# Performance work log

Hardware: AMD Instinct MI355X
Metric: run time of the kernel (lower is better)

Reference implementation:

```python
import jax, jax.numpy as jnp
import numpy as np

N, E, VD, HD, ES = 10000, 80000, 32, 64, 68
NET_IN = VD * VD + 2 * HD + ES   # 1220: f2s(1024) + s[e0](64) + s[e1](64) + edge_s(68)
SELF_IN = VD * VD + 2 * HD       # 1152: temp_f2s(1024) + s(64) + s_c(64)
OUT_D = VD * VD + HD             # 1088: vector channel mixer + scalar update


def _lecun(k, fin, fout):
    return jax.random.normal(k, (fin, fout), jnp.float32) / jnp.sqrt(jnp.float32(fin))


def setup_inputs() -> dict:
    ks = jax.random.split(jax.random.key(0), 16)
    return {
        "f": jax.random.normal(ks[0], (N, 3, VD), jnp.float32),
        "s": jax.random.normal(ks[1], (N, HD), jnp.float32),
        "edge_f": jax.random.normal(ks[2], (E, 3, 1), jnp.float32),
        "edge_s": jax.random.normal(ks[3], (E, ES), jnp.float32),
        "W_emb1": _lecun(ks[4], 2 * VD + 1, VD),
        "net_W1": _lecun(ks[5], NET_IN, HD), "net_b1": jnp.zeros((HD,), jnp.float32),
        "net_W2": _lecun(ks[6], HD, HD), "net_b2": jnp.zeros((HD,), jnp.float32),
        "net_W3": _lecun(ks[7], HD, OUT_D), "net_b3": jnp.zeros((OUT_D,), jnp.float32),
        "W_emb2": _lecun(ks[8], 2 * VD, VD),
        "self_W1": _lecun(ks[9], SELF_IN, HD), "self_b1": jnp.zeros((HD,), jnp.float32),
        "self_W2": _lecun(ks[10], HD, HD), "self_b2": jnp.zeros((HD,), jnp.float32),
        "self_W3": _lecun(ks[11], HD, OUT_D), "self_b3": jnp.zeros((OUT_D,), jnp.float32),
        "edge_index": jax.random.randint(ks[12], (2, E), 0, N),
    }


def _mlp(x, W1, b1, W2, b2, W3, b3):
    h = jax.nn.relu(x @ W1 + b1)
    h = jax.nn.relu(h @ W2 + b2)
    return h @ W3 + b3


def _segment_mean(x, ids, n):
    tot = jax.ops.segment_sum(x, ids, num_segments=n)
    cnt = jax.ops.segment_sum(jnp.ones(ids.shape, x.dtype), ids, num_segments=n)
    return tot / jnp.maximum(cnt, 1.0).reshape((n,) + (1,) * (x.ndim - 1))


def _forward(f, s, edge_f, edge_s,
             W_emb1, net_W1, net_b1, net_W2, net_b2, net_W3, net_b3,
             W_emb2, self_W1, self_b1, self_W2, self_b2, self_W3, self_b3,
             edge_index):
    n = f.shape[0]
    e0, e1 = edge_index[0], edge_index[1]
    # --- edge message: gather -> embed -> gram einsum -> MLP ---
    _f = jnp.concatenate((f[e0], f[e1], edge_f), axis=-1)          # [E,3,2VD+1]
    _s = jnp.concatenate((s[e0], s[e1], edge_s), axis=-1)          # [E,2HD+ES]
    _f = _f @ W_emb1                                               # [E,3,VD]
    f2s = jnp.einsum('eij,eik->ejk', _f, _f).reshape(-1, VD * VD)  # _f^T @ _f, [E,VD*VD]
    Fn = jnp.linalg.norm(f2s, axis=-1, keepdims=True) + 1.0
    c = _mlp(jnp.concatenate((f2s, _s), axis=-1),
             net_W1, net_b1, net_W2, net_b2, net_W3, net_b3) / Fn  # [E,OUT_D]
    f_c = jnp.einsum('eij,ejk->eik', _f, c[:, :VD * VD].reshape(-1, VD, VD))  # [E,3,VD]
    f_c = _segment_mean(f_c, e0, n)                                # [N,3,VD]
    s_c = _segment_mean(c[:, VD * VD:], e0, n)                     # [N,HD]
    # --- node self-update ---
    tf = jnp.concatenate((f, f_c), axis=-1) @ W_emb2               # [N,3,VD]
    tf2s = jnp.einsum('nij,nik->njk', tf, tf).reshape(n, VD * VD)
    Fn2 = jnp.linalg.norm(tf2s, axis=-1, keepdims=True) + 1.0
    c2 = _mlp(jnp.concatenate((tf2s, s, s_c), axis=-1),
              self_W1, self_b1, self_W2, self_b2, self_W3, self_b3) / Fn2
    f_out = jnp.einsum('nij,njk->nik', tf, c2[:, :VD * VD].reshape(-1, VD, VD)) + f
    s_out = c2[:, VD * VD:] + s
    return f_out, s_out


def reference(f, s, edge_f, edge_s,
              W_emb1, net_W1, net_b1, net_W2, net_b2, net_W3, net_b3,
              W_emb2, self_W1, self_b1, self_W2, self_b2, self_W3, self_b3,
              edge_index):
    return _forward(f, s, edge_f, edge_s,
                    W_emb1, net_W1, net_b1, net_W2, net_b2, net_W3, net_b3,
                    W_emb2, self_W1, self_b1, self_W2, self_b2, self_W3, self_b3,
                    edge_index)
```

## Files before the change

### kernel.cpp

```cpp
#include <hip/hip_runtime.h>
#include <math.h>

#define NN 10000
#define NE 80000
#define SFH 102
#define SFB 98
#define SSB 66
#define STX 72
#define NTRI 528
#define SAE 104
#define SAN 72

typedef __attribute__((ext_vector_type(8))) __bf16 bf16x8;
typedef __attribute__((ext_vector_type(8))) short short8v;
typedef __attribute__((ext_vector_type(4))) float f32x4;
typedef __attribute__((ext_vector_type(4))) unsigned uint4v;

__device__ __forceinline__ ushort f2bf(float x) {
  union { float f; unsigned u; } v; v.f = x;
  unsigned r = v.u + 0x7FFFu + ((v.u >> 16) & 1u);
  return (ushort)(r >> 16);
}
__device__ __forceinline__ float bfu(ushort u) {
  union { unsigned x; float f; } v; v.x = (unsigned)u << 16;
  return v.f;
}
__device__ __forceinline__ void tri_ab(int k, int& a, int& b) {
  int aa = 0, rem = k;
  while (rem >= 32 - aa) { rem -= 32 - aa; ++aa; }
  a = aa; b = aa + rem;
}

__global__ __launch_bounds__(1024)
void sgnn_scan(const int* __restrict__ deg, int* __restrict__ cursor,
               int* __restrict__ start) {
  __shared__ int sm[1024];
  const int t = threadIdx.x;
  const int i0 = t * 10;
  int v[10], pre = 0;
  #pragma unroll
  for (int q = 0; q < 10; ++q) {
    const int i = i0 + q;
    v[q] = (i < NN) ? deg[i] : 0;
    pre += v[q];
  }
  sm[t] = pre;
  __syncthreads();
  int run = pre;
  #pragma unroll
  for (int d = 1; d < 1024; d <<= 1) {
    const int add = (t >= d) ? sm[t - d] : 0;
    __syncthreads();
    run += add;
    sm[t] = run;
    __syncthreads();
  }
  int excl = run - pre;
  #pragma unroll
  for (int q = 0; q < 10; ++q) {
    const int i = i0 + q;
    if (i < NN) { cursor[i] = excl; start[i] = excl; }
    excl += v[q];
  }
}

__global__ __launch_bounds__(256)
void sgnn_scatter(const int* __restrict__ eidx, int* __restrict__ cursor,
                  int* __restrict__ sorted) {
  const int e = blockIdx.x * 256 + threadIdx.x;
  if (e < NE) {
    const int p = atomicAdd(cursor + eidx[e], 1);
    sorted[p] = e;
  }
}

__global__ __launch_bounds__(256)
void sgnn_wconv(const float* __restrict__ nW1, const float* __restrict__ nW2,
                const float* __restrict__ nW3, const float* __restrict__ sW1,
                const float* __restrict__ sW2, const float* __restrict__ sW3,
                const float* __restrict__ Wemb1, const float* __restrict__ Wemb2,
                const int* __restrict__ eidx, int* __restrict__ deg,
                ushort* __restrict__ wout, ushort* __restrict__ tab) {
  const int gid = blockIdx.x * 256 + threadIdx.x;
  if (gid < NE) atomicAdd(deg + eidx[gid], 1);
  if (gid >= 61 * 4096) {
    const int k = gid - 61 * 4096;
    if (k < NTRI) {
      int a, b; tri_ab(k, a, b);
      tab[k] = (ushort)(a | (b << 8) | ((a != b) ? 0x8000 : 0));
    }
    return;
  }
  const int tile = gid >> 12, idx = gid & 4095;
  const int c = idx >> 6, k = idx & 63;
  float v = 0.f;
  if (tile < 12) {
    const int T = tile;
    if (T < 8 || (T == 8 && k < 16)) {
      const int ktri = T * 64 + k;
      if (ktri < NTRI) {
        int a, b; tri_ab(ktri, a, b);
        v = nW1[(a * 32 + b) * 64 + c];
        if (a != b) v += nW1[(b * 32 + a) * 64 + c];
      }
    } else if (T == 8) { if (k < 20) v = nW1[(1216 + (k - 16)) * 64 + c]; }
    else if (T == 9)   v = nW1[(1024 + k) * 64 + c];
    else if (T == 10)  v = nW1[(1088 + k) * 64 + c];
    else               v = nW1[(1152 + k) * 64 + c];
  } else if (tile == 12) v = nW2[k * 64 + c];
  else if (tile < 30)    v = nW3[k * 1088 + (tile - 13) * 64 + c];
  else if (tile < 41) {
    const int T = tile - 30;
    if (T < 8 || (T == 8 && k < 16)) {
      const int ktri = T * 64 + k;
      if (ktri < NTRI) {
        int a, b; tri_ab(ktri, a, b);
        v = sW1[(a * 32 + b) * 64 + c];
        if (a != b) v += sW1[(b * 32 + a) * 64 + c];
      }
    } else if (T == 9) v = sW1[(1024 + k) * 64 + c];
    else if (T == 10)  v = sW1[(1088 + k) * 64 + c];
  } else if (tile == 41) v = sW2[k * 64 + c];
  else if (tile < 59)    v = sW3[k * 1088 + (tile - 42) * 64 + c];
  else if (tile == 59) {
    const int col = idx / 96, kk = idx % 96;
    v = (col < 32 && kk < 65) ? Wemb1[kk * 32 + col] : 0.f;
  } else {
    const int col = idx >> 6;
    v = (col < 32) ? Wemb2[k * 32 + col] : 0.f;
  }
  wout[gid] = f2bf(v);
}

#define STAGE_W(srcbase) do { const ushort* _s = (srcbase);                      \
  _Pragma("unroll") for (int rr = 0; rr < 2; ++rr) {                             \
    const int idx_ = t + 256 * rr; const int c_ = idx_ >> 3, ko_ = idx_ & 7;     \
    *(short8v*)&Wl[c_ * STX + ko_ * 8] = *(const short8v*)&_s[c_ * 64 + ko_ * 8];\
  } } while (0)

#define WPRE_LOAD(srcbase) do { const ushort* _s = (srcbase);                    \
  wpre0 = *(const short8v*)&_s[(t >> 3) * 64 + (t & 7) * 8];                     \
  wpre1 = *(const short8v*)&_s[(32 + (t >> 3)) * 64 + (t & 7) * 8]; } while (0)

#define WPRE_STORE() do {                                                        \
  *(short8v*)&Wl[(t >> 3) * STX + (t & 7) * 8] = wpre0;                          \
  *(short8v*)&Wl[(32 + (t >> 3)) * STX + (t & 7) * 8] = wpre1; } while (0)

#define MFMA_K64() do {                                                          \
  _Pragma("unroll") for (int kb = 0; kb < 2; ++kb) {                             \
    const bf16x8 af_ = *(const bf16x8*)&Xl[(w * 16 + ll) * STX + kb * 32 + lh * 8]; \
    acc[0] = __builtin_amdgcn_mfma_f32_16x16x32_bf16(af_,                        \
        *(const bf16x8*)&Wl[(     ll) * STX + kb * 32 + lh * 8], acc[0], 0, 0, 0); \
    acc[1] = __builtin_amdgcn_mfma_f32_16x16x32_bf16(af_,                        \
        *(const bf16x8*)&Wl[(16 + ll) * STX + kb * 32 + lh * 8], acc[1], 0, 0, 0); \
    acc[2] = __builtin_amdgcn_mfma_f32_16x16x32_bf16(af_,                        \
        *(const bf16x8*)&Wl[(32 + ll) * STX + kb * 32 + lh * 8], acc[2], 0, 0, 0); \
    acc[3] = __builtin_amdgcn_mfma_f32_16x16x32_bf16(af_,                        \
        *(const bf16x8*)&Wl[(48 + ll) * STX + kb * 32 + lh * 8], acc[3], 0, 0, 0); \
  } } while (0)

#define ZERO_ACC() do { _Pragma("unroll") for (int q = 0; q < 4; ++q)            \
    acc[q] = (f32x4){0.f, 0.f, 0.f, 0.f}; } while (0)

#define PACK_STORE16(dstp) do {                                                  \
  unsigned pk[8];                                                                \
  _Pragma("unroll") for (int q = 0; q < 8; ++q)                                  \
    pk[q] = (unsigned)f2bf(xv[2 * q]) | ((unsigned)f2bf(xv[2 * q + 1]) << 16);   \
  *(uint4v*)(dstp)       = (uint4v){pk[0], pk[1], pk[2], pk[3]};                 \
  *(uint4v*)((dstp) + 8) = (uint4v){pk[4], pk[5], pk[6], pk[7]};                 \
} while (0)

#define TRI16(kt) do {                                                           \
  int prev_a = -1; float fa0 = 0.f, fa1 = 0.f, fa2 = 0.f;                        \
  _Pragma("unroll") for (int m = 0; m < 16; ++m) {                               \
    const int tb = tabL[(kt) + m];                                               \
    const int a_ = tb & 31, b_ = (tb >> 8) & 31;                                 \
    if (a_ != prev_a) { fa0 = bfu(fr[a_]); fa1 = bfu(fr[32 + a_]);               \
                        fa2 = bfu(fr[64 + a_]); prev_a = a_; }                   \
    const float v = fmaf(fa0, bfu(fr[b_]),                                       \
        fmaf(fa1, bfu(fr[32 + b_]), fa2 * bfu(fr[64 + b_])));                    \
    const float wsel = (tb & 0x8000) ? 2.f : 1.f;                                \
    sumsq = fmaf(v * wsel, v, sumsq);                                            \
    xv[m] = v;                                                                   \
  } } while (0)

#define XV_LOAD16(p) do { const float* _p = (p);                                 \
  _Pragma("unroll") for (int q = 0; q < 4; ++q) {                                \
    const float4 v4 = *(const float4*)(_p + 4 * q);                              \
    xv[4 * q + 0] = v4.x; xv[4 * q + 1] = v4.y;                                  \
    xv[4 * q + 2] = v4.z; xv[4 * q + 3] = v4.w; } } while (0)

#define CONSUME_NT() do {                                                        \
  _Pragma("unroll") for (int r = 0; r < 4; ++r) {                                \
    const int row_ = w * 16 + lh * 4 + r;                                        \
    const unsigned u0 = *(const unsigned*)&smFh[row_ * SFH +      nt * 2];       \
    const unsigned u1 = *(const unsigned*)&smFh[row_ * SFH + 32 + nt * 2];       \
    const unsigned u2 = *(const unsigned*)&smFh[row_ * SFH + 64 + nt * 2];       \
    union { unsigned x; float f; } l0, h0, l1, h1, l2, h2;                       \
    l0.x = u0 << 16; h0.x = u0 & 0xffff0000u;                                    \
    l1.x = u1 << 16; h1.x = u1 & 0xffff0000u;                                    \
    l2.x = u2 << 16; h2.x = u2 & 0xffff0000u;                                    \
    _Pragma("unroll") for (int nc = 0; nc < 4; ++nc) {                           \
      const float cv = (acc[nc][r] + b3v[nc]) * ifnr[r];                         \
      const int p = nc & 1;                                                      \
      const float f0 = (nc < 2) ? l0.f : h0.f;                                   \
      const float f1 = (nc < 2) ? l1.f : h1.f;                                   \
      const float f2 = (nc < 2) ? l2.f : h2.f;                                   \
      fch[(r * 3 + 0) * 2 + p] = fmaf(f0, cv, fch[(r * 3 + 0) * 2 + p]);         \
      fch[(r * 3 + 1) * 2 + p] = fmaf(f1, cv, fch[(r * 3 + 1) * 2 + p]);         \
      fch[(r * 3 + 2) * 2 + p] = fmaf(f2, cv, fch[(r * 3 + 2) * 2 + p]);         \
    }                                                                            \
  } } while (0)

#define STAGE_FS() do {                                                          \
  _Pragma("unroll") for (int r = 0; r < 4; ++r) {                                \
    const int row_ = w * 16 + lh * 4 + r;                                        \
    _Pragma("unroll") for (int i = 0; i < 3; ++i) {                              \
      F[row_ * SFB + i * 32 + ll]      = f2bf(fch[(r * 3 + i) * 2 + 0]);         \
      F[row_ * SFB + i * 32 + ll + 16] = f2bf(fch[(r * 3 + i) * 2 + 1]);         \
    }                                                                            \
    _Pragma("unroll") for (int nc = 0; nc < 4; ++nc)                             \
      S[row_ * SSB + nc * 16 + ll] = f2bf(cs[nc * 4 + r]);                       \
  } } while (0)

#define LDS_BYTES 34656

__global__ __launch_bounds__(256, 3)
void sgnn_edge(const float* __restrict__ f, const float* __restrict__ s,
               const float* __restrict__ edge_f, const float* __restrict__ edge_s,
               const float* __restrict__ b1, const float* __restrict__ b2,
               const float* __restrict__ b3,
               const ushort* __restrict__ wbf, const ushort* __restrict__ tab_g,
               const int* __restrict__ eidx, const int* __restrict__ sorted,
               const int* __restrict__ start_g, const int* __restrict__ deg_g,
               float* __restrict__ fc_sum, float* __restrict__ sc_sum) {
  __shared__ __align__(16) char sbuf[LDS_BYTES];
  ushort* smFh = (ushort*)sbuf;
  ushort* F    = (ushort*)sbuf;
  ushort* Xl   = (ushort*)(sbuf + 13056);
  ushort* S    = (ushort*)(sbuf + 13056);
  ushort* Aemb = (ushort*)(sbuf + 13056);
  ushort* Wl   = (ushort*)(sbuf + 22272);
  float*  red  = (float*)(sbuf + 31488);
  int*    snode = (int*)(sbuf + 31488);
  int*    srow0 = snode + 8;
  int*    srow1 = snode + 16;
  int*    sst   = snode + 24;
  int*    sdg   = snode + 32;
  ushort* tabL = (ushort*)(sbuf + 33088);
  float*  iFn  = (float*)(sbuf + 33088);
  int*    es_s = (int*)(sbuf + 34144);
  ushort* e0s  = (ushort*)(sbuf + 34400);
  ushort* e1s  = (ushort*)(sbuf + 34528);

  const int t = threadIdx.x, j = t & 63, w = t >> 6, eb = w * 16;
  const int lh = j >> 4, ll = j & 15;
  const int bid = blockIdx.x;
  const ushort* wembT = wbf + 59 * 4096;
  short8v wpre0, wpre1;

  if (t < 64) {
    const int e = sorted[bid * 64 + t];
    es_s[t] = e;
    e0s[t] = (ushort)eidx[e];
    e1s[t] = (ushort)eidx[NE + e];
  }
  for (int idx = t; idx < NTRI; idx += 256) tabL[idx] = tab_g[idx];
  __syncthreads();

  int str = 0, dgr = 0;
  if (j < 16) {
    const int n_ = e0s[eb + j];
    str = start_g[n_];
    dgr = deg_g[n_];
  }
  WPRE_LOAD(wbf + 0);

  #pragma unroll 1
  for (int h = 0; h < 2; ++h) {
    const int hb = h * 32;
    #pragma unroll 1
    for (int cc = t; cc < 576; cc += 256) {
      const int row = cc / 6, seg = cc - row * 6;
      const int lel = (row * 43) >> 7, il = row - lel * 3;
      const int k0 = seg * 16;
      float xv[16];
      if (seg < 4) {
        const int nd = (seg < 2) ? (int)e0s[hb + lel] : (int)e1s[hb + lel];
        XV_LOAD16(f + nd * 96 + il * 32 + (seg & 1) * 16);
      } else if (seg == 4) {
        xv[0] = edge_f[es_s[hb + lel] * 3 + il];
        #pragma unroll
        for (int m = 1; m < 16; ++m) xv[m] = 0.f;
      } else {
        #pragma unroll
        for (int m = 0; m < 16; ++m) xv[m] = 0.f;
      }
      PACK_STORE16(&Aemb[row * SAE + k0]);
    }
    __syncthreads();
    #pragma unroll 1
    for (int job = w * 3; job < w * 3 + 3; ++job) {
      const int mt = job >> 1, nt = job & 1;
      f32x4 ac = (f32x4){0.f, 0.f, 0.f, 0.f};
      #pragma unroll
      for (int kb = 0; kb < 3; ++kb) {
        const bf16x8 av = *(const bf16x8*)&Aemb[(mt * 16 + ll) * SAE + kb * 32 + lh * 8];
        const bf16x8 bv = *(const bf16x8*)&wembT[(nt * 16 + ll) * 96 + kb * 32 + lh * 8];
        ac = __builtin_amdgcn_mfma_f32_16x16x32_bf16(av, bv, ac, 0, 0, 0);
      }
      #pragma unroll
      for (int r = 0; r < 4; ++r) {
        const int rr = mt * 16 + lh * 4 + r;
        const int lel = (rr * 43) >> 7, il = rr - lel * 3;
        smFh[(hb + lel) * SFH + il * 32 + nt * 16 + ll] = f2bf(ac[r]);
      }
    }
    __syncthreads();
  }

  f32x4 acc[4];
  ZERO_ACC();
  float sumsq = 0.f;

  #pragma unroll 1
  for (int T = 0; T < 12; ++T) {
    __syncthreads();
    WPRE_STORE();
    {
      const ushort* fr = smFh + j * SFH;
      float xv[16];
      if (T < 8) {
        TRI16(T * 64 + w * 16);
      } else if (T == 8) {
        if (w == 0) {
          TRI16(512);
        } else if (w == 1) {
          const float4 v4 = *(const float4*)(edge_s + es_s[j] * 68 + 64);
          xv[0] = v4.x; xv[1] = v4.y; xv[2] = v4.z; xv[3] = v4.w;
          #pragma unroll
          for (int m = 4; m < 16; ++m) xv[m] = 0.f;
        } else {
          #pragma unroll
          for (int m = 0; m < 16; ++m) xv[m] = 0.f;
        }
      } else if (T == 9)  { XV_LOAD16(s + e0s[j] * 64 + w * 16); }
      else if (T == 10)   { XV_LOAD16(s + e1s[j] * 64 + w * 16); }
      else                { XV_LOAD16(edge_s + es_s[j] * 68 + w * 16); }
      PACK_STORE16(&Xl[j * STX + w * 16]);
    }
    __syncthreads();
    WPRE_LOAD(wbf + (T + 1) * 4096);
    MFMA_K64();
  }

  __syncthreads();
  red[w * 64 + j] = sumsq;
  #pragma unroll
  for (int nc = 0; nc < 4; ++nc) {
    const float bv = b1[nc * 16 + ll];
    #pragma unroll
    for (int r = 0; r < 4; ++r)
      Xl[(w * 16 + lh * 4 + r) * STX + nc * 16 + ll] = f2bf(fmaxf(acc[nc][r] + bv, 0.f));
  }
  WPRE_STORE();
  ZERO_ACC();
  __syncthreads();
  if (t < 64) {
    const float ss = red[t] + red[64 + t] + red[128 + t] + red[192 + t];
    iFn[t] = 1.f / (sqrtf(ss) + 1.f);
  }

  MFMA_K64();
  #pragma unroll
  for (int nc = 0; nc < 4; ++nc) {
    const float bv = b2[nc * 16 + ll];
    #pragma unroll
    for (int r = 0; r < 4; ++r)
      Xl[(w * 16 + lh * 4 + r) * STX + nc * 16 + ll] = f2bf(fmaxf(acc[nc][r] + bv, 0.f));
  }

  float fch[24];
  #pragma unroll
  for (int q = 0; q < 24; ++q) fch[q] = 0.f;
  float cs[16];
  float ifnr[4];

  #pragma unroll 1
  for (int nt = 0; nt < 17; ++nt) {
    __syncthreads();
    STAGE_W(wbf + (13 + nt) * 4096);
    float b3v[4];
    #pragma unroll
    for (int nc = 0; nc < 4; ++nc) b3v[nc] = b3[nt * 64 + nc * 16 + ll];
    __syncthreads();
    if (nt == 0) {
      #pragma unroll
      for (int r = 0; r < 4; ++r) ifnr[r] = iFn[w * 16 + lh * 4 + r];
    }
    ZERO_ACC();
    MFMA_K64();
    if (nt < 16) {
      CONSUME_NT();
    } else {
      #pragma unroll
      for (int nc = 0; nc < 4; ++nc)
        #pragma unroll
        for (int r = 0; r < 4; ++r)
          cs[nc * 4 + r] = (acc[nc][r] + b3v[nc]) * ifnr[r];
    }
  }

  __syncthreads();
  STAGE_FS();
  if (t < 8) snode[t] = -1;
  __syncthreads();

  {
    float r0 = 0.f, r1 = 0.f, rs = 0.f;
    int runlen = 0;
    const int gwb = bid * 64 + eb;
    #pragma unroll 1
    for (int m = 0; m < 16; ++m) {
      const int row = eb + m;
      r0 += bfu(F[row * SFB + j]);
      if (j < 32) r1 += bfu(F[row * SFB + 64 + j]);
      rs += bfu(S[row * SSB + j]);
      ++runlen;
      const int n = e0s[row];
      if (m == 15 || e0s[row + 1] != n) {
        const int st = __shfl(str, m);
        const int dg = __shfl(dgr, m);
        const int g1v = gwb + m, g0v = g1v - runlen + 1;
        if (g0v == st && runlen == dg) {
          fc_sum[n * 96 + j] = r0;
          if (j < 32) fc_sum[n * 96 + 64 + j] = r1;
          sc_sum[n * 64 + j] = rs;
        } else {
          const int slot = (g0v == gwb) ? 2 * w : 2 * w + 1;
          if (j == 0) {
            snode[slot] = n; srow0[slot] = row - runlen + 1; srow1[slot] = row;
            sst[slot] = st; sdg[slot] = dg;
          }
        }
        r0 = r1 = rs = 0.f; runlen = 0;
      }
    }
  }
  __syncthreads();

  if (t < 160) {
    const int ch = t;
    int prevn = -1;
    #pragma unroll 1
    for (int ss = 0; ss < 8; ++ss) {
      const int n = snode[ss];
      if (n < 0) continue;
      if (n != prevn) {
        float v = 0.f;
        #pragma unroll 1
        for (int k2 = ss; k2 < 8; ++k2) {
          if (snode[k2] == n) {
            #pragma unroll 1
            for (int row = srow0[k2]; row <= srow1[k2]; ++row)
              v += (ch < 96) ? bfu(F[row * SFB + ch]) : bfu(S[row * SSB + (ch - 96)]);
          } else if (k2 > ss && snode[k2] >= 0) break;
        }
        const bool cib = (sst[ss] >= bid * 64) && (sst[ss] + sdg[ss] <= bid * 64 + 64);
        float* dst = (ch < 96) ? (fc_sum + n * 96 + ch) : (sc_sum + n * 64 + (ch - 96));
        if (cib) *dst = v; else atomicAdd(dst, v);
      }
      prevn = n;
    }
  }
}

__global__ __launch_bounds__(256, 3)
void sgnn_node(const float* __restrict__ f, const float* __restrict__ s,
               const float* __restrict__ b1, const float* __restrict__ b2,
               const float* __restrict__ b3,
               const ushort* __restrict__ wbf, const ushort* __restrict__ tab_g,
               const float* __restrict__ fcm, const float* __restrict__ scm,
               const int* __restrict__ deg_g,
               float* __restrict__ of, float* __restrict__ os) {
  __shared__ __align__(16) char sbuf[LDS_BYTES];
  ushort* smFh = (ushort*)sbuf;
  ushort* F    = (ushort*)sbuf;
  ushort* Xl   = (ushort*)(sbuf + 13056);
  ushort* S    = (ushort*)(sbuf + 13056);
  ushort* Aemb = (ushort*)(sbuf + 13056);
  ushort* Wl   = (ushort*)(sbuf + 22272);
  float*  red  = (float*)(sbuf + 31488);
  float*  icntL = (float*)(sbuf + 31488);
  ushort* tabL = (ushort*)(sbuf + 33088);
  float*  iFn  = (float*)(sbuf + 33088);

  const int t = threadIdx.x, j = t & 63, w = t >> 6, eb = w * 16;
  const int lh = j >> 4, ll = j & 15;
  const int nbase = blockIdx.x * 64;
  const ushort* wembTn = wbf + 60 * 4096;
  short8v wpre0, wpre1;

  for (int idx = t; idx < NTRI; idx += 256) tabL[idx] = tab_g[idx];
  if (t < 64)
    icntL[t] = 1.f / fmaxf((float)deg_g[min(nbase + t, NN - 1)], 1.f);
  WPRE_LOAD(wbf + 30 * 4096);
  __syncthreads();

  #pragma unroll 1
  for (int h = 0; h < 2; ++h) {
    const int hb = h * 32;
    #pragma unroll 1
    for (int cc = t; cc < 384; cc += 256) {
      const int row = cc >> 2, seg = cc & 3;
      const int lel = (row * 43) >> 7, il = row - lel * 3;
      const int nc = min(nbase + hb + lel, NN - 1);
      const int k0 = seg * 16;
      float xv[16];
      if (seg < 2) {
        XV_LOAD16(f + nc * 96 + il * 32 + seg * 16);
      } else {
        XV_LOAD16(fcm + nc * 96 + il * 32 + (seg - 2) * 16);
        const float ic = icntL[hb + lel];
        #pragma unroll
        for (int m = 0; m < 16; ++m) xv[m] *= ic;
      }
      PACK_STORE16(&Aemb[row * SAN + k0]);
    }
    __syncthreads();
    #pragma unroll 1
    for (int job = w * 3; job < w * 3 + 3; ++job) {
      const int mt = job >> 1, nt = job & 1;
      f32x4 ac = (f32x4){0.f, 0.f, 0.f, 0.f};
      #pragma unroll
      for (int kb = 0; kb < 2; ++kb) {
        const bf16x8 av = *(const bf16x8*)&Aemb[(mt * 16 + ll) * SAN + kb * 32 + lh * 8];
        const bf16x8 bv = *(const bf16x8*)&wembTn[(nt * 16 + ll) * 64 + kb * 32 + lh * 8];
        ac = __builtin_amdgcn_mfma_f32_16x16x32_bf16(av, bv, ac, 0, 0, 0);
      }
      #pragma unroll
      for (int r = 0; r < 4; ++r) {
        const int rr = mt * 16 + lh * 4 + r;
        const int lel = (rr * 43) >> 7, il = rr - lel * 3;
        smFh[(hb + lel) * SFH + il * 32 + nt * 16 + ll] = f2bf(ac[r]);
      }
    }
    __syncthreads();
  }

  f32x4 acc[4];
  ZERO_ACC();
  float sumsq = 0.f;

  #pragma unroll 1
  for (int T = 0; T < 11; ++T) {
    __syncthreads();
    WPRE_STORE();
    {
      const ushort* fr = smFh + j * SFH;
      float xv[16];
      if (T < 8) {
        TRI16(T * 64 + w * 16);
      } else if (T == 8) {
        if (w == 0) {
          TRI16(512);
        } else {
          #pragma unroll
          for (int m = 0; m < 16; ++m) xv[m] = 0.f;
        }
      } else if (T == 9) {
        XV_LOAD16(s + min(nbase + j, NN - 1) * 64 + w * 16);
      } else {
        XV_LOAD16(scm + min(nbase + j, NN - 1) * 64 + w * 16);
        const float ic = icntL[j];
        #pragma unroll
        for (int m = 0; m < 16; ++m) xv[m] *= ic;
      }
      PACK_STORE16(&Xl[j * STX + w * 16]);
    }
    __syncthreads();
    WPRE_LOAD(wbf + (31 + T) * 4096);
    MFMA_K64();
  }

  __syncthreads();
  red[w * 64 + j] = sumsq;
  #pragma unroll
  for (int nc = 0; nc < 4; ++nc) {
    const float bv = b1[nc * 16 + ll];
    #pragma unroll
    for (int r = 0; r < 4; ++r)
      Xl[(w * 16 + lh * 4 + r) * STX + nc * 16 + ll] = f2bf(fmaxf(acc[nc][r] + bv, 0.f));
  }
  WPRE_STORE();
  ZERO_ACC();
  __syncthreads();
  if (t < 64) {
    const float ss = red[t] + red[64 + t] + red[128 + t] + red[192 + t];
    iFn[t] = 1.f / (sqrtf(ss) + 1.f);
  }

  MFMA_K64();
  #pragma unroll
  for (int nc = 0; nc < 4; ++nc) {
    const float bv = b2[nc * 16 + ll];
    #pragma unroll
    for (int r = 0; r < 4; ++r)
      Xl[(w * 16 + lh * 4 + r) * STX + nc * 16 + ll] = f2bf(fmaxf(acc[nc][r] + bv, 0.f));
  }

  float fch[24];
  #pragma unroll
  for (int q = 0; q < 24; ++q) fch[q] = 0.f;
  float cs[16];
  float ifnr[4];

  #pragma unroll 1
  for (int nt = 0; nt < 17; ++nt) {
    __syncthreads();
    STAGE_W(wbf + (42 + nt) * 4096);
    float b3v[4];
    #pragma unroll
    for (int nc = 0; nc < 4; ++nc) b3v[nc] = b3[nt * 64 + nc * 16 + ll];
    __syncthreads();
    if (nt == 0) {
      #pragma unroll
      for (int r = 0; r < 4; ++r) ifnr[r] = iFn[w * 16 + lh * 4 + r];
    }
    ZERO_ACC();
    MFMA_K64();
    if (nt < 16) {
      CONSUME_NT();
    } else {
      #pragma unroll
      for (int nc = 0; nc < 4; ++nc)
        #pragma unroll
        for (int r = 0; r < 4; ++r)
          cs[nc * 4 + r] = (acc[nc][r] + b3v[nc]) * ifnr[r];
    }
  }

  __syncthreads();
  STAGE_FS();
  __syncthreads();

  #pragma unroll 1
  for (int m = 0; m < 16; ++m) {
    const int row = eb + m;
    const int n_m = nbase + row;
    if (n_m < NN) {
      of[n_m * 96 + j] = bfu(F[row * SFB + j]) + f[n_m * 96 + j];
      if (j < 32)
        of[n_m * 96 + 64 + j] = bfu(F[row * SFB + 64 + j]) + f[n_m * 96 + 64 + j];
      os[n_m * 64 + j] = bfu(S[row * SSB + j]) + s[n_m * 64 + j];
    }
  }
}

extern "C" void kernel_launch(void* const* d_in, const int* in_sizes, int n_in,
                              void* d_out, int out_size, void* d_ws, size_t ws_size,
                              hipStream_t stream) {
  const float* f      = (const float*)d_in[0];
  const float* s      = (const float*)d_in[1];
  const float* edge_f = (const float*)d_in[2];
  const float* edge_s = (const float*)d_in[3];
  const float* Wemb1  = (const float*)d_in[4];
  const float* nW1 = (const float*)d_in[5];
  const float* nb1 = (const float*)d_in[6];
  const float* nW2 = (const float*)d_in[7];
  const float* nb2 = (const float*)d_in[8];
  const float* nW3 = (const float*)d_in[9];
  const float* nb3 = (const float*)d_in[10];
  const float* Wemb2 = (const float*)d_in[11];
  const float* sW1 = (const float*)d_in[12];
  const float* sb1 = (const float*)d_in[13];
  const float* sW2 = (const float*)d_in[14];
  const float* sb2 = (const float*)d_in[15];
  const float* sW3 = (const float*)d_in[16];
  const float* sb3 = (const float*)d_in[17];
  const int* eidx  = (const int*)d_in[18];

  float* of = (float*)d_out;
  float* os = of + (size_t)NN * 96;

  int* deg    = (int*)d_ws;
  int* cursor = deg + NN;
  int* start  = cursor + NN;
  int* sorted = start + NN;
  ushort* wbf = (ushort*)(sorted + NE);
  ushort* tab = wbf + 61 * 4096;

  hipMemsetAsync(deg, 0, (size_t)NN * 4, stream);
  hipMemsetAsync(d_out, 0, (size_t)NN * 160 * 4, stream);

  hipLaunchKernelGGL(sgnn_wconv, dim3((61 * 4096 + NTRI + 255) / 256), dim3(256),
                     0, stream, nW1, nW2, nW3, sW1, sW2, sW3, Wemb1, Wemb2,
                     eidx, deg, wbf, tab);
  hipLaunchKernelGGL(sgnn_scan, dim3(1), dim3(1024), 0, stream, deg, cursor, start);
  hipLaunchKernelGGL(sgnn_scatter, dim3((NE + 255) / 256), dim3(256), 0, stream,
                     eidx, cursor, sorted);
  hipLaunchKernelGGL(sgnn_edge, dim3(NE / 64), dim3(256), 0, stream,
                     f, s, edge_f, edge_s, nb1, nb2, nb3,
                     wbf, tab, eidx, sorted, start, deg,
                     of , os );
  hipLaunchKernelGGL(sgnn_node, dim3((NN + 63) / 64), dim3(256), 0, stream,
                     f, s, sb1, sb2, sb3,
                     wbf, tab, of , os , deg, of, os);
}
```

Baseline: 202.3 us.

## Build MFMA A-operands in registers and prefetch layer-3 weights

In both the edge and node kernels, each lane now computes the gram features for exactly the slots of its MFMA A-fragment and packs them straight into bf16x8 registers. This drops the per-tile store of activations to the Xl shared-memory tile and the reads back from it. The sum-of-squares reduction for the norm becomes a wave shuffle instead of a shared-memory reduction. The third-layer weight staging switches from synchronous STAGE_W to register prefetch (WPRE_LOAD/STORE) one tile ahead, so global weight loads overlap the MFMAs. The cost is higher register pressure at launch bounds of 3 blocks per SM, and recomputation of the repeated frA loads.

```diff
diff --git a/kernel.cpp b/kernel.cpp
--- a/kernel.cpp
+++ b/kernel.cpp
@@ -146,6 +146,25 @@
   *(short8v*)&Wl[(t >> 3) * STX + (t & 7) * 8] = wpre0;                          \
   *(short8v*)&Wl[(32 + (t >> 3)) * STX + (t & 7) * 8] = wpre1; } while (0)
 
+#define MFMA_K64_RA() do {                                                       \
+  acc[0] = __builtin_amdgcn_mfma_f32_16x16x32_bf16(af0.v8,                       \
+      *(const bf16x8*)&Wl[(     ll) * STX + lh * 8], acc[0], 0, 0, 0);           \
+  acc[1] = __builtin_amdgcn_mfma_f32_16x16x32_bf16(af0.v8,                       \
+      *(const bf16x8*)&Wl[(16 + ll) * STX + lh * 8], acc[1], 0, 0, 0);           \
+  acc[2] = __builtin_amdgcn_mfma_f32_16x16x32_bf16(af0.v8,                       \
+      *(const bf16x8*)&Wl[(32 + ll) * STX + lh * 8], acc[2], 0, 0, 0);           \
+  acc[3] = __builtin_amdgcn_mfma_f32_16x16x32_bf16(af0.v8,                       \
+      *(const bf16x8*)&Wl[(48 + ll) * STX + lh * 8], acc[3], 0, 0, 0);           \
+  acc[0] = __builtin_amdgcn_mfma_f32_16x16x32_bf16(af1.v8,                       \
+      *(const bf16x8*)&Wl[(     ll) * STX + 32 + lh * 8], acc[0], 0, 0, 0);      \
+  acc[1] = __builtin_amdgcn_mfma_f32_16x16x32_bf16(af1.v8,                       \
+      *(const bf16x8*)&Wl[(16 + ll) * STX + 32 + lh * 8], acc[1], 0, 0, 0);      \
+  acc[2] = __builtin_amdgcn_mfma_f32_16x16x32_bf16(af1.v8,                       \
+      *(const bf16x8*)&Wl[(32 + ll) * STX + 32 + lh * 8], acc[2], 0, 0, 0);      \
+  acc[3] = __builtin_amdgcn_mfma_f32_16x16x32_bf16(af1.v8,                       \
+      *(const bf16x8*)&Wl[(48 + ll) * STX + 32 + lh * 8], acc[3], 0, 0, 0);      \
+} while (0)
+
 #define MFMA_K64() do {                                                          \
   _Pragma("unroll") for (int kb = 0; kb < 2; ++kb) {                             \
     const bf16x8 af_ = *(const bf16x8*)&Xl[(w * 16 + ll) * STX + kb * 32 + lh * 8]; \
@@ -170,19 +189,32 @@
   *(uint4v*)((dstp) + 8) = (uint4v){pk[4], pk[5], pk[6], pk[7]};                 \
 } while (0)
 
-#define TRI16(kt) do {                                                           \
+#define PACK_AF() do {                                                           \
+  _Pragma("unroll") for (int q2 = 0; q2 < 4; ++q2) {                             \
+    af0.u[q2] = (unsigned)f2bf(xv[2 * q2]) | ((unsigned)f2bf(xv[2 * q2 + 1]) << 16); \
+    af1.u[q2] = (unsigned)f2bf(xv[8 + 2 * q2]) | ((unsigned)f2bf(xv[8 + 2 * q2 + 1]) << 16); \
+  } } while (0)
+
+#define TRI8(kt, off) do {                                                       \
   int prev_a = -1; float fa0 = 0.f, fa1 = 0.f, fa2 = 0.f;                        \
-  _Pragma("unroll") for (int m = 0; m < 16; ++m) {                               \
-    const int tb = tabL[(kt) + m];                                               \
+  _Pragma("unroll") for (int q = 0; q < 8; ++q) {                                \
+    const int tb = tabL[(kt) + q];                                               \
     const int a_ = tb & 31, b_ = (tb >> 8) & 31;                                 \
-    if (a_ != prev_a) { fa0 = bfu(fr[a_]); fa1 = bfu(fr[32 + a_]);               \
-                        fa2 = bfu(fr[64 + a_]); prev_a = a_; }                   \
-    const float v = fmaf(fa0, bfu(fr[b_]),                                       \
-        fmaf(fa1, bfu(fr[32 + b_]), fa2 * bfu(fr[64 + b_])));                    \
+    if (a_ != prev_a) { fa0 = bfu(frA[a_]); fa1 = bfu(frA[32 + a_]);             \
+                        fa2 = bfu(frA[64 + a_]); prev_a = a_; }                  \
+    const float v = fmaf(fa0, bfu(frA[b_]),                                      \
+        fmaf(fa1, bfu(frA[32 + b_]), fa2 * bfu(frA[64 + b_])));                  \
     const float wsel = (tb & 0x8000) ? 2.f : 1.f;                                \
     sumsq = fmaf(v * wsel, v, sumsq);                                            \
-    xv[m] = v;                                                                   \
+    xv[(off) + q] = v;                                                           \
   } } while (0)
+
+#define XV8_LOAD(p, off) do { const float* _p = (p);                             \
+  const float4 va = *(const float4*)(_p);                                        \
+  const float4 vb = *(const float4*)(_p + 4);                                    \
+  xv[(off)+0]=va.x; xv[(off)+1]=va.y; xv[(off)+2]=va.z; xv[(off)+3]=va.w;        \
+  xv[(off)+4]=vb.x; xv[(off)+5]=vb.y; xv[(off)+6]=vb.z; xv[(off)+7]=vb.w;        \
+} while (0)
 
 #define XV_LOAD16(p) do { const float* _p = (p);                                 \
   _Pragma("unroll") for (int q = 0; q < 4; ++q) {                                \
@@ -241,7 +273,6 @@
   ushort* S    = (ushort*)(sbuf + 13056);
   ushort* Aemb = (ushort*)(sbuf + 13056);
   ushort* Wl   = (ushort*)(sbuf + 22272);
-  float*  red  = (float*)(sbuf + 31488);
   int*    snode = (int*)(sbuf + 31488);
   int*    srow0 = snode + 8;
   int*    srow1 = snode + 16;
@@ -322,40 +353,58 @@
   f32x4 acc[4];
   ZERO_ACC();
   float sumsq = 0.f;
+  const int rowA = w * 16 + ll;
+  const ushort* frA = smFh + rowA * SFH;
 
   #pragma unroll 1
   for (int T = 0; T < 12; ++T) {
+    float xv[16];
+    union { unsigned u[4]; bf16x8 v8; } af0, af1;
+    if (T < 8) {
+      TRI8(T * 64 + lh * 8, 0);
+      TRI8(T * 64 + 32 + lh * 8, 8);
+    } else if (T == 8) {
+      #pragma unroll
+      for (int kb2 = 0; kb2 < 2; ++kb2)
+        #pragma unroll
+        for (int q = 0; q < 8; ++q) {
+          const int k = kb2 * 32 + lh * 8 + q;
+          float v = 0.f;
+          if (k < 16) {
+            const int tb = tabL[512 + k];
+            const int a_ = tb & 31, b_ = (tb >> 8) & 31;
+            v = fmaf(bfu(frA[a_]), bfu(frA[b_]),
+                fmaf(bfu(frA[32 + a_]), bfu(frA[32 + b_]),
+                     bfu(frA[64 + a_]) * bfu(frA[64 + b_])));
+            const float wsel = (tb & 0x8000) ? 2.f : 1.f;
+            sumsq = fmaf(v * wsel, v, sumsq);
+          } else if (k < 20) {
+            v = edge_s[es_s[rowA] * 68 + 64 + (k - 16)];
+          }
+          xv[kb2 * 8 + q] = v;
+        }
+    } else {
+      const float* p = (T == 9)  ? (s + e0s[rowA] * 64)
+                     : (T == 10) ? (s + e1s[rowA] * 64)
+                                 : (edge_s + es_s[rowA] * 68);
+      XV8_LOAD(p + lh * 8, 0);
+      XV8_LOAD(p + 32 + lh * 8, 8);
+    }
+    PACK_AF();
     __syncthreads();
     WPRE_STORE();
-    {
-      const ushort* fr = smFh + j * SFH;
-      float xv[16];
-      if (T < 8) {
-        TRI16(T * 64 + w * 16);
-      } else if (T == 8) {
-        if (w == 0) {
-          TRI16(512);
-        } else if (w == 1) {
-          const float4 v4 = *(const float4*)(edge_s + es_s[j] * 68 + 64);
-          xv[0] = v4.x; xv[1] = v4.y; xv[2] = v4.z; xv[3] = v4.w;
-          #pragma unroll
-          for (int m = 4; m < 16; ++m) xv[m] = 0.f;
-        } else {
-          #pragma unroll
-          for (int m = 0; m < 16; ++m) xv[m] = 0.f;
-        }
-      } else if (T == 9)  { XV_LOAD16(s + e0s[j] * 64 + w * 16); }
-      else if (T == 10)   { XV_LOAD16(s + e1s[j] * 64 + w * 16); }
-      else                { XV_LOAD16(edge_s + es_s[j] * 68 + w * 16); }
-      PACK_STORE16(&Xl[j * STX + w * 16]);
-    }
     __syncthreads();
     WPRE_LOAD(wbf + (T + 1) * 4096);
-    MFMA_K64();
-  }
-
-  __syncthreads();
-  red[w * 64 + j] = sumsq;
+    MFMA_K64_RA();
+  }
+
+  {
+    float ss = sumsq;
+    ss += __shfl_xor(ss, 16);
+    ss += __shfl_xor(ss, 32);
+    __syncthreads();
+    if (j < 16) iFn[eb + j] = 1.f / (sqrtf(ss) + 1.f);
+  }
   #pragma unroll
   for (int nc = 0; nc < 4; ++nc) {
     const float bv = b1[nc * 16 + ll];
@@ -366,10 +415,7 @@
   WPRE_STORE();
   ZERO_ACC();
   __syncthreads();
-  if (t < 64) {
-    const float ss = red[t] + red[64 + t] + red[128 + t] + red[192 + t];
-    iFn[t] = 1.f / (sqrtf(ss) + 1.f);
-  }
+  WPRE_LOAD(wbf + 13 * 4096);
 
   MFMA_K64();
   #pragma unroll
@@ -389,11 +435,12 @@
   #pragma unroll 1
   for (int nt = 0; nt < 17; ++nt) {
     __syncthreads();
-    STAGE_W(wbf + (13 + nt) * 4096);
+    WPRE_STORE();
     float b3v[4];
     #pragma unroll
     for (int nc = 0; nc < 4; ++nc) b3v[nc] = b3[nt * 64 + nc * 16 + ll];
     __syncthreads();
+    if (nt < 16) WPRE_LOAD(wbf + (14 + nt) * 4096);
     if (nt == 0) {
       #pragma unroll
       for (int r = 0; r < 4; ++r) ifnr[r] = iFn[w * 16 + lh * 4 + r];
@@ -490,7 +537,6 @@
   ushort* S    = (ushort*)(sbuf + 13056);
   ushort* Aemb = (ushort*)(sbuf + 13056);
   ushort* Wl   = (ushort*)(sbuf + 22272);
-  float*  red  = (float*)(sbuf + 31488);
   float*  icntL = (float*)(sbuf + 31488);
   ushort* tabL = (ushort*)(sbuf + 33088);
   float*  iFn  = (float*)(sbuf + 33088);
@@ -551,40 +597,60 @@
   f32x4 acc[4];
   ZERO_ACC();
   float sumsq = 0.f;
+  const int rowA = w * 16 + ll;
+  const ushort* frA = smFh + rowA * SFH;
+  const int ncA = min(nbase + rowA, NN - 1);
 
   #pragma unroll 1
   for (int T = 0; T < 11; ++T) {
+    float xv[16];
+    union { unsigned u[4]; bf16x8 v8; } af0, af1;
+    if (T < 8) {
+      TRI8(T * 64 + lh * 8, 0);
+      TRI8(T * 64 + 32 + lh * 8, 8);
+    } else if (T == 8) {
+      #pragma unroll
+      for (int kb2 = 0; kb2 < 2; ++kb2)
+        #pragma unroll
+        for (int q = 0; q < 8; ++q) {
+          const int k = kb2 * 32 + lh * 8 + q;
+          float v = 0.f;
+          if (k < 16) {
+            const int tb = tabL[512 + k];
+            const int a_ = tb & 31, b_ = (tb >> 8) & 31;
+            v = fmaf(bfu(frA[a_]), bfu(frA[b_]),
+                fmaf(bfu(frA[32 + a_]), bfu(frA[32 + b_]),
+                     bfu(frA[64 + a_]) * bfu(frA[64 + b_])));
+            const float wsel = (tb & 0x8000) ? 2.f : 1.f;
+            sumsq = fmaf(v * wsel, v, sumsq);
+          }
+          xv[kb2 * 8 + q] = v;
+        }
+    } else if (T == 9) {
+      XV8_LOAD(s + ncA * 64 + lh * 8, 0);
+      XV8_LOAD(s + ncA * 64 + 32 + lh * 8, 8);
+    } else {
+      const float ic = icntL[rowA];
+      XV8_LOAD(scm + ncA * 64 + lh * 8, 0);
+      XV8_LOAD(scm + ncA * 64 + 32 + lh * 8, 8);
+      #pragma unroll
+      for (int m = 0; m < 16; ++m) xv[m] *= ic;
+    }
+    PACK_AF();
     __syncthreads();
     WPRE_STORE();
-    {
-      const ushort* fr = smFh + j * SFH;
-      float xv[16];
-      if (T < 8) {
-        TRI16(T * 64 + w * 16);
-      } else if (T == 8) {
-        if (w == 0) {
-          TRI16(512);
-        } else {
-          #pragma unroll
-          for (int m = 0; m < 16; ++m) xv[m] = 0.f;
-        }
-      } else if (T == 9) {
-        XV_LOAD16(s + min(nbase + j, NN - 1) * 64 + w * 16);
-      } else {
-        XV_LOAD16(scm + min(nbase + j, NN - 1) * 64 + w * 16);
-        const float ic = icntL[j];
-        #pragma unroll
-        for (int m = 0; m < 16; ++m) xv[m] *= ic;
-      }
-      PACK_STORE16(&Xl[j * STX + w * 16]);
-    }
     __syncthreads();
     WPRE_LOAD(wbf + (31 + T) * 4096);
-    MFMA_K64();
-  }
-
-  __syncthreads();
-  red[w * 64 + j] = sumsq;
+    MFMA_K64_RA();
+  }
+
+  {
+    float ss = sumsq;
+    ss += __shfl_xor(ss, 16);
+    ss += __shfl_xor(ss, 32);
+    __syncthreads();
+    if (j < 16) iFn[eb + j] = 1.f / (sqrtf(ss) + 1.f);
+  }
   #pragma unroll
   for (int nc = 0; nc < 4; ++nc) {
     const float bv = b1[nc * 16 + ll];
@@ -595,10 +661,7 @@
   WPRE_STORE();
   ZERO_ACC();
   __syncthreads();
-  if (t < 64) {
-    const float ss = red[t] + red[64 + t] + red[128 + t] + red[192 + t];
-    iFn[t] = 1.f / (sqrtf(ss) + 1.f);
-  }
+  WPRE_LOAD(wbf + 42 * 4096);
 
   MFMA_K64();
   #pragma unroll
@@ -618,11 +681,12 @@
   #pragma unroll 1
   for (int nt = 0; nt < 17; ++nt) {
     __syncthreads();
-    STAGE_W(wbf + (42 + nt) * 4096);
+    WPRE_STORE();
     float b3v[4];
     #pragma unroll
     for (int nc = 0; nc < 4; ++nc) b3v[nc] = b3[nt * 64 + nc * 16 + ll];
     __syncthreads();
+    if (nt < 16) WPRE_LOAD(wbf + (43 + nt) * 4096);
     if (nt == 0) {
       #pragma unroll
       for (int r = 0; r < 4; ++r) ifnr[r] = iFn[w * 16 + lh * 4 + r];
```

Measured after the change: 198.0 us. 1.02x faster.
